# Kernel tuning notes

Hardware: AMD Instinct MI355X
Metric: run time of the kernel (lower is better)

## Reference

```python
import jax, jax.numpy as jnp
import numpy as np

# dims
B, T = 128, 1024
INP, HUMAN = 54, 64          # input_dim, output_dim (HUMAN_SIZE)
DEC, ENC = 256, 256          # decoder / encoder GRU sizes
K, H_PSI, LR_PSI = 16, 256, 32
N_PSI = DEC*DEC + DEC + DEC*INP + DEC*HUMAN + INP*(HUMAN-INP)  # 96540


def setup_inputs() -> dict:
    key = jax.random.key(0)
    ks = jax.random.split(key, 16)
    g = lambda i, shape, s=0.05: jax.random.normal(ks[i], shape, jnp.float32) * s
    return {
        "inputs": g(0, (B, T, INP), 1.0),
        "state": jnp.zeros((B, DEC), jnp.float32),
        "eps": g(1, (B, K), 1.0),
        # encoder GRUCell params (torch gate order r,z,n)
        "enc_Wih": g(2, (3*ENC, INP)),
        "enc_Whh": g(3, (3*ENC, ENC)),
        "enc_bih": jnp.zeros((3*ENC,), jnp.float32),
        "enc_bhh": jnp.zeros((3*ENC,), jnp.float32),
        # latent projections
        "to_mu": g(4, (K, ENC)),
        "to_lsigma": g(5, (K, ENC)),
        # psi hypernetwork MLP
        "W1": g(6, (H_PSI, K)),   "b1": jnp.zeros((H_PSI,), jnp.float32),
        "W2": g(7, (LR_PSI, H_PSI)), "b2": jnp.zeros((LR_PSI,), jnp.float32),
        "W3": g(8, (N_PSI, LR_PSI), 0.01), "b3": jnp.zeros((N_PSI,), jnp.float32),
        # shared decoder gate params (bias second half init to ones, as in module)
        "gru_Wih": g(9, (2*DEC, INP)),
        "gru_Whh": g(10, (DEC, 2*DEC)),
        "gru_bias": jnp.concatenate([jnp.zeros((DEC,)), jnp.ones((DEC,))]).astype(jnp.float32),
    }


def reference(inputs, state, eps, enc_Wih, enc_Whh, enc_bih, enc_bhh,
              to_mu, to_lsigma, W1, b1, W2, b2, W3, b3,
              gru_Wih, gru_Whh, gru_bias):
    x_tbd = jnp.swapaxes(inputs, 0, 1)  # [T,B,INP]

    # ---- encoder GRU scan (torch GRUCell semantics) ----
    def enc_step(h, x_t):
        gi = x_t @ enc_Wih.T + enc_bih
        gh = h @ enc_Whh.T + enc_bhh
        ir, iz, inn = jnp.split(gi, 3, axis=-1)
        hr, hz, hn = jnp.split(gh, 3, axis=-1)
        r = jax.nn.sigmoid(ir + hr)
        z = jax.nn.sigmoid(iz + hz)
        n = jnp.tanh(inn + r * hn)
        return (1 - z) * n + z * h, None

    h_enc, _ = jax.lax.scan(enc_step, jnp.zeros((inputs.shape[0], ENC), inputs.dtype), x_tbd)

    # ---- MT latent ----
    mu = h_enc @ to_mu.T                 # [B,K]
    logstd = h_enc @ to_lsigma.T         # [B,K]
    z_lat = mu + eps * jnp.exp(logstd)

    # ---- psi hypernetwork ----
    psi = jnp.tanh(z_lat @ W1.T + b1) @ W2.T + b2
    psi = psi @ W3.T + b3                # [B, N_PSI]

    o = 0
    Whh_p = psi[:, o:o+DEC*DEC].reshape(-1, DEC, DEC); o += DEC*DEC
    bh_p  = psi[:, o:o+DEC];                           o += DEC
    Wih_p = psi[:, o:o+DEC*INP].reshape(-1, DEC, INP); o += DEC*INP
    C_p   = psi[:, o:o+DEC*HUMAN].reshape(-1, DEC, HUMAN); o += DEC*HUMAN
    D_p   = psi[:, o:o+INP*(HUMAN-INP)].reshape(-1, INP, HUMAN-INP)

    # ---- per-sample hypernet-weighted GRU decoder, vectorized over batch ----
    def dec_step(h, x_t):  # h:[B,DEC], x_t:[B,INP]
        gx = x_t @ gru_Wih.T                       # [B,2*DEC]
        gh = h @ gru_Whh                           # [B,2*DEC]
        zt = jax.nn.sigmoid(gx[:, :DEC] + gh[:, :DEC] + gru_bias[:DEC])
        rt = jax.nn.sigmoid(gx[:, DEC:] + gh[:, DEC:] + gru_bias[DEC:])
        eta = jnp.tanh(jnp.einsum('bd,bhd->bh', x_t, Wih_p)
                       + rt * jnp.tanh(jnp.einsum('bh,bhg->bg', h, Whh_p) + bh_p))
        h_new = zt * h + (1 - zt) * eta
        return h_new, h_new

    h_last, dec_seq = jax.lax.scan(dec_step, state, x_tbd)
    dec_seq = jnp.swapaxes(dec_seq, 0, 1)          # [B,T,DEC]

    # yhat = dec@C + cat(zeros, x@D) ; residual adds inputs to first INP cols
    yD = jnp.einsum('btd,bde->bte', inputs, D_p)   # [B,T,HUMAN-INP]
    yhats = jnp.einsum('bth,bho->bto', dec_seq, C_p) + jnp.concatenate([inputs, yD], axis=-1)

    return yhats, mu, logstd, h_last
```

## Files before the change

### kernel.cpp

```cpp
#include <hip/hip_runtime.h>

#define BB 128
#define TT 1024
#define INP 54
#define HUM 64
#define NPSI 96540
#define OFF_BH 65536
#define OFF_WIH 65792
#define OFF_C 79616
#define OFF_D 96000
#define OUT_MU 8388608
#define OUT_LS 8390656
#define OUT_HL 8392704

typedef unsigned int u32;
typedef unsigned short u16;
typedef _Float16 h2 __attribute__((ext_vector_type(2)));

__device__ __forceinline__ u32 pk(float a, float b) {
    h2 v; v.x = (_Float16)a; v.y = (_Float16)b;
    return __builtin_bit_cast(u32, v);
}
__device__ __forceinline__ float f16tof(u16 v) {
    return (float)__builtin_bit_cast(_Float16, v);
}
__device__ __forceinline__ u16 ftof16(float v) {
    return __builtin_bit_cast(u16, (_Float16)v);
}
__device__ __forceinline__ float lo16f(u32 v) { return f16tof((u16)(v & 0xffffu)); }
__device__ __forceinline__ float hi16f(u32 v) { return f16tof((u16)(v >> 16)); }
__device__ __forceinline__ h2 bch2(u32 a) { return __builtin_bit_cast(h2, a); }
__device__ __forceinline__ float fd2(u32 a, u32 b, float c) {
#if __has_builtin(__builtin_amdgcn_fdot2)
    return __builtin_amdgcn_fdot2(bch2(a), bch2(b), c, false);
#else
    return c + lo16f(a) * lo16f(b) + hi16f(a) * hi16f(b);
#endif
}
__device__ __forceinline__ float fsig(float x) { return 1.f / (1.f + __expf(-x)); }
__device__ __forceinline__ float ftanh(float x) { float e = __expf(2.f * x); return 1.f - 2.f / (e + 1.f); }

__device__ __forceinline__ float qred(float v) {
#if __has_builtin(__builtin_amdgcn_mov_dpp)
    int x = __builtin_bit_cast(int, v);
    v += __builtin_bit_cast(float, __builtin_amdgcn_mov_dpp(x, 0xB1, 0xF, 0xF, true));
    x = __builtin_bit_cast(int, v);
    v += __builtin_bit_cast(float, __builtin_amdgcn_mov_dpp(x, 0x4E, 0xF, 0xF, true));
    return v;
#else
    v += __shfl_xor(v, 1); v += __shfl_xor(v, 2);
    return v;
#endif
}

__global__ __launch_bounds__(768, 3) void gemm_x_kernel(
    const float* __restrict__ inp, const float* __restrict__ W0,
    const u16* __restrict__ psi16, int mode, int t0, int len, int ct, int nt,
    u16* __restrict__ gout)
{
    const int tid = threadIdx.x;
    const int b = blockIdx.x / nt, tc = blockIdx.x % nt;
    const int gr = tid;
    float w[INP];
    if (mode == 0 || gr < 512) {
        const float* wsrc = W0 + (size_t)gr * INP;
#pragma unroll
        for (int c = 0; c < INP; ++c) w[c] = wsrc[c];
    } else {
        const u16* wsrc = psi16 + (size_t)b * NPSI + OFF_WIH + (size_t)(gr - 512) * INP;
#pragma unroll
        for (int c = 0; c < INP; ++c) w[c] = f16tof(wsrc[c]);
    }
    const int tb = tc * 128;
    const int te = (tb + 128 < len) ? tb + 128 : len;
    for (int tl = tb; tl < te; ++tl) {
        const float* xr = inp + ((size_t)b * TT + t0 + tl) * INP;
        float a = 0.f;
#pragma unroll
        for (int c = 0; c < INP; ++c) a = __builtin_fmaf(xr[c], w[c], a);
        gout[((size_t)b * ct + tl) * 768 + gr] = ftof16(a);
    }
}

__global__ __launch_bounds__(512) __attribute__((amdgpu_waves_per_eu(2, 2)))
void enc_scan_kernel(
    const u16* __restrict__ gi, int t0, int len, int ct,
    const float* __restrict__ Whh, const float* __restrict__ bih,
    const float* __restrict__ bhh, float* __restrict__ hcarry)
{
    __shared__ __align__(16) u32 hpp[2][144];
    const int tid = threadIdx.x, b = blockIdx.x;
    const int l = tid & 3, g = tid >> 2;
    const int j0 = 2 * g, j1 = 2 * g + 1;

    u32 wr0[32], wz0[32], wn0[32], wr1[32], wz1[32], wn1[32];
    {
        const float* pr0 = Whh + (size_t)j0 * 256 + 64 * l;
        const float* pz0 = Whh + (size_t)(256 + j0) * 256 + 64 * l;
        const float* pn0 = Whh + (size_t)(512 + j0) * 256 + 64 * l;
        const float* pr1 = Whh + (size_t)j1 * 256 + 64 * l;
        const float* pz1 = Whh + (size_t)(256 + j1) * 256 + 64 * l;
        const float* pn1 = Whh + (size_t)(512 + j1) * 256 + 64 * l;
#pragma unroll
        for (int c = 0; c < 32; ++c) {
            wr0[c] = pk(pr0[2 * c], pr0[2 * c + 1]);
            wz0[c] = pk(pz0[2 * c], pz0[2 * c + 1]);
            wn0[c] = pk(pn0[2 * c], pn0[2 * c + 1]);
            wr1[c] = pk(pr1[2 * c], pr1[2 * c + 1]);
            wz1[c] = pk(pz1[2 * c], pz1[2 * c + 1]);
            wn1[c] = pk(pn1[2 * c], pn1[2 * c + 1]);
        }
    }
    const float brb0 = bih[j0] + bhh[j0],             brb1 = bih[j1] + bhh[j1];
    const float bzb0 = bih[256 + j0] + bhh[256 + j0], bzb1 = bih[256 + j1] + bhh[256 + j1];
    const float bib0 = bih[512 + j0],                 bib1 = bih[512 + j1];
    const float bhb0 = bhh[512 + j0],                 bhb1 = bhh[512 + j1];
    float hc0 = 0.f, hc1 = 0.f;
    if (t0 > 0) { hc0 = hcarry[(size_t)b * 256 + j0]; hc1 = hcarry[(size_t)b * 256 + j1]; }
    if (tid < 128) {
        u32 hv = 0u;
        if (t0 > 0) hv = pk(hcarry[(size_t)b * 256 + 2 * tid], hcarry[(size_t)b * 256 + 2 * tid + 1]);
        hpp[0][36 * (tid >> 5) + (tid & 31)] = hv;
    }
    __syncthreads();

    const u16* gbase = gi + (size_t)b * ct * 768;
    u32 c0 = *(const u32*)(gbase + 2 * g);
    u32 c1 = *(const u32*)(gbase + 256 + 2 * g);
    u32 c2 = *(const u32*)(gbase + 512 + 2 * g);

    for (int tl = 0; tl < len; ++tl) {
        const int p = tl & 1;
        u32 n0 = 0, n1 = 0, n2 = 0;
        if (tl + 1 < len) {
            const u16* gn = gbase + (size_t)(tl + 1) * 768;
            n0 = *(const u32*)(gn + 2 * g);
            n1 = *(const u32*)(gn + 256 + 2 * g);
            n2 = *(const u32*)(gn + 512 + 2 * g);
        }
        float ar0 = 0, az0 = 0, ah0 = 0, ar1 = 0, az1 = 0, ah1 = 0;
        const uint4* hq = (const uint4*)hpp[p];
#pragma unroll
        for (int cc = 0; cc < 8; ++cc) {
            uint4 q = hq[9 * l + cc];
            u32 qa[4] = {q.x, q.y, q.z, q.w};
#pragma unroll
            for (int u = 0; u < 4; ++u) {
                const int c = cc * 4 + u;
                ar0 = fd2(wr0[c], qa[u], ar0);
                az0 = fd2(wz0[c], qa[u], az0);
                ah0 = fd2(wn0[c], qa[u], ah0);
                ar1 = fd2(wr1[c], qa[u], ar1);
                az1 = fd2(wz1[c], qa[u], az1);
                ah1 = fd2(wn1[c], qa[u], ah1);
            }
        }
        ar0 = qred(ar0); az0 = qred(az0); ah0 = qred(ah0);
        ar1 = qred(ar1); az1 = qred(az1); ah1 = qred(ah1);
        {
            float r0 = fsig(ar0 + lo16f(c0) + brb0);
            float z0 = fsig(az0 + lo16f(c1) + bzb0);
            float nn0 = ftanh(lo16f(c2) + bib0 + r0 * (ah0 + bhb0));
            float hn0 = (1.f - z0) * nn0 + z0 * hc0;
            float r1 = fsig(ar1 + hi16f(c0) + brb1);
            float z1 = fsig(az1 + hi16f(c1) + bzb1);
            float nn1 = ftanh(hi16f(c2) + bib1 + r1 * (ah1 + bhb1));
            float hn1 = (1.f - z1) * nn1 + z1 * hc1;
            hc0 = hn0; hc1 = hn1;
            if (l == 0) hpp[p ^ 1][36 * (g >> 5) + (g & 31)] = pk(hn0, hn1);
        }
        c0 = n0; c1 = n1; c2 = n2;
        __syncthreads();
    }
    if (l == 0) {
        hcarry[(size_t)b * 256 + j0] = hc0;
        hcarry[(size_t)b * 256 + j1] = hc1;
    }
}

__global__ __launch_bounds__(256) void latent_kernel(
    const float* __restrict__ henc, const float* __restrict__ eps,
    const float* __restrict__ to_mu, const float* __restrict__ to_ls,
    const float* __restrict__ W1, const float* __restrict__ b1,
    const float* __restrict__ W2, const float* __restrict__ b2,
    float* __restrict__ psi2, float* __restrict__ out)
{
    __shared__ float h[256], zz[16], p1[256];
    const int tid = threadIdx.x, b = blockIdx.x;
    h[tid] = henc[(size_t)b * 256 + tid];
    __syncthreads();
    if (tid < 16) {
        float m = 0, s = 0;
        for (int k = 0; k < 256; ++k) {
            m += h[k] * to_mu[tid * 256 + k];
            s += h[k] * to_ls[tid * 256 + k];
        }
        out[OUT_MU + b * 16 + tid] = m;
        out[OUT_LS + b * 16 + tid] = s;
        zz[tid] = m + eps[b * 16 + tid] * __expf(s);
    }
    __syncthreads();
    {
        float a = b1[tid];
        for (int k = 0; k < 16; ++k) a += zz[k] * W1[tid * 16 + k];
        p1[tid] = ftanh(a);
    }
    __syncthreads();
    if (tid < 32) {
        float a = b2[tid];
        for (int k = 0; k < 256; ++k) a += p1[k] * W2[tid * 256 + k];
        psi2[b * 32 + tid] = a;
    }
}

__global__ __launch_bounds__(256) void psi3_kernel(
    const float* __restrict__ psi2, const float* __restrict__ W3,
    const float* __restrict__ b3, u16* __restrict__ psi16)
{
    __shared__ float sp2[128 * 32];
    __shared__ float w3t[256 * 33];
    const int tid = threadIdx.x;
    const int n0 = blockIdx.x * 256;
    for (int idx = tid; idx < 4096; idx += 256) sp2[idx] = psi2[idx];
    for (int idx = tid; idx < 8192; idx += 256) {
        int row = idx >> 5, k = idx & 31;
        int n = n0 + row;
        w3t[row * 33 + k] = (n < NPSI) ? W3[(size_t)n * 32 + k] : 0.f;
    }
    __syncthreads();
    const int n = n0 + tid;
    if (n < NPSI) {
        float w[32];
#pragma unroll
        for (int k = 0; k < 32; ++k) w[k] = w3t[tid * 33 + k];
        const float bv = b3[n];
        for (int bi = 0; bi < 128; ++bi) {
            float a = bv;
#pragma unroll
            for (int k = 0; k < 32; ++k) a += sp2[bi * 32 + k] * w[k];
            psi16[(size_t)bi * NPSI + n] = ftof16(a);
        }
    }
}

__global__ __launch_bounds__(512) __attribute__((amdgpu_waves_per_eu(2, 2)))
void dec_scan_kernel(
    const u16* __restrict__ gx, int t0, int len, int ct,
    const float* __restrict__ state, const float* __restrict__ gWhh,
    const float* __restrict__ gbias, const u16* __restrict__ psi16,
    float* __restrict__ dcarry, float* __restrict__ out)
{
    __shared__ __align__(16) u32 hpp[2][144];
    __shared__ u32 cp[64 * 129];
    __shared__ float part[2][8 * 64];
    const int tid = threadIdx.x, b = blockIdx.x;
    const int l = tid & 3, g = tid >> 2;
    const int j0 = 2 * g, j1 = 2 * g + 1;
    const u16* pc = psi16 + (size_t)b * NPSI;

    u32 wz0[32], wr0[32], wp0[32], wz1[32], wr1[32], wp1[32];
#pragma unroll
    for (int c = 0; c < 32; ++c) {
        const int h0 = 64 * l + 2 * c;
        wz0[c] = pk(gWhh[(size_t)h0 * 512 + j0], gWhh[(size_t)(h0 + 1) * 512 + j0]);
        wr0[c] = pk(gWhh[(size_t)h0 * 512 + 256 + j0], gWhh[(size_t)(h0 + 1) * 512 + 256 + j0]);
        wp0[c] = (u32)pc[(size_t)h0 * 256 + j0] | ((u32)pc[(size_t)(h0 + 1) * 256 + j0] << 16);
        wz1[c] = pk(gWhh[(size_t)h0 * 512 + j1], gWhh[(size_t)(h0 + 1) * 512 + j1]);
        wr1[c] = pk(gWhh[(size_t)h0 * 512 + 256 + j1], gWhh[(size_t)(h0 + 1) * 512 + 256 + j1]);
        wp1[c] = (u32)pc[(size_t)h0 * 256 + j1] | ((u32)pc[(size_t)(h0 + 1) * 256 + j1] << 16);
    }
    const float gzb0 = gbias[j0], gzb1 = gbias[j1];
    const float grb0 = gbias[256 + j0], grb1 = gbias[256 + j1];
    const float bhb0 = f16tof(pc[OFF_BH + j0]), bhb1 = f16tof(pc[OFF_BH + j1]);
    for (int idx = tid; idx < 8192; idx += 512) {
        const int q = idx >> 6, o = idx & 63;
        cp[o * 129 + q] = (u32)pc[OFF_C + (size_t)(2 * q) * 64 + o]
                        | ((u32)pc[OFF_C + (size_t)(2 * q + 1) * 64 + o] << 16);
    }
    const float* hsrc = (t0 == 0) ? state : dcarry;
    float hc0 = hsrc[(size_t)b * 256 + j0];
    float hc1 = hsrc[(size_t)b * 256 + j1];
    if (tid < 128) hpp[0][36 * (tid >> 5) + (tid & 31)] =
        pk(hsrc[(size_t)b * 256 + 2 * tid], hsrc[(size_t)b * 256 + 2 * tid + 1]);
    __syncthreads();

    const u16* gbase = gx + (size_t)b * ct * 768;
    const int o = tid & 63, s = tid >> 6;
    const int hqi = 36 * (s >> 1) + 16 * (s & 1);
    u32 c0 = *(const u32*)(gbase + 2 * g);
    u32 c1 = *(const u32*)(gbase + 256 + 2 * g);
    u32 c2 = *(const u32*)(gbase + 512 + 2 * g);

    for (int tl = 0; tl < len; ++tl) {
        const int p = tl & 1;
        u32 n0 = 0, n1 = 0, n2 = 0;
        if (tl + 1 < len) {
            const u16* gn = gbase + (size_t)(tl + 1) * 768;
            n0 = *(const u32*)(gn + 2 * g);
            n1 = *(const u32*)(gn + 256 + 2 * g);
            n2 = *(const u32*)(gn + 512 + 2 * g);
        }
        {
            const uint4* h2q = (const uint4*)&hpp[p][hqi];
            uint4 qa = h2q[0], qb = h2q[1], qc = h2q[2], qd = h2q[3];
            u32 hv[16] = {qa.x, qa.y, qa.z, qa.w, qb.x, qb.y, qb.z, qb.w,
                          qc.x, qc.y, qc.z, qc.w, qd.x, qd.y, qd.z, qd.w};
            const int cbase = o * 129 + s * 16;
            float p0 = 0.f, p1 = 0.f;
#pragma unroll
            for (int i = 0; i < 8; ++i) {
                p0 = fd2(hv[2 * i], cp[cbase + 2 * i], p0);
                p1 = fd2(hv[2 * i + 1], cp[cbase + 2 * i + 1], p1);
            }
            part[p][s * 64 + o] = p0 + p1;
        }
        float az0 = 0, ar0 = 0, ap0 = 0, az1 = 0, ar1 = 0, ap1 = 0;
        const uint4* hq = (const uint4*)hpp[p];
#pragma unroll
        for (int cc = 0; cc < 8; ++cc) {
            uint4 q = hq[9 * l + cc];
            u32 qa[4] = {q.x, q.y, q.z, q.w};
#pragma unroll
            for (int u = 0; u < 4; ++u) {
                const int c = cc * 4 + u;
                az0 = fd2(wz0[c], qa[u], az0);
                ar0 = fd2(wr0[c], qa[u], ar0);
                ap0 = fd2(wp0[c], qa[u], ap0);
                az1 = fd2(wz1[c], qa[u], az1);
                ar1 = fd2(wr1[c], qa[u], ar1);
                ap1 = fd2(wp1[c], qa[u], ap1);
            }
        }
        az0 = qred(az0); ar0 = qred(ar0); ap0 = qred(ap0);
        az1 = qred(az1); ar1 = qred(ar1); ap1 = qred(ap1);
        {
            float zt0 = fsig(az0 + lo16f(c0) + gzb0);
            float rt0 = fsig(ar0 + lo16f(c1) + grb0);
            float eta0 = ftanh(lo16f(c2) + rt0 * ftanh(ap0 + bhb0));
            float hn0 = zt0 * hc0 + (1.f - zt0) * eta0;
            float zt1 = fsig(az1 + hi16f(c0) + gzb1);
            float rt1 = fsig(ar1 + hi16f(c1) + grb1);
            float eta1 = ftanh(hi16f(c2) + rt1 * ftanh(ap1 + bhb1));
            float hn1 = zt1 * hc1 + (1.f - zt1) * eta1;
            hc0 = hn0; hc1 = hn1;
            if (l == 0) hpp[p ^ 1][36 * (g >> 5) + (g & 31)] = pk(hn0, hn1);
        }
        if (tid < 64 && tl >= 2) {
            float y = 0.f;
#pragma unroll
            for (int s2 = 0; s2 < 8; ++s2) y += part[p ^ 1][s2 * 64 + tid];
            out[((size_t)b * TT + t0 + tl - 2) * HUM + tid] = y;
        }
        c0 = n0; c1 = n1; c2 = n2;
        __syncthreads();
    }
    {
        const int pf = (len - 1) & 1;
        if (tid < 64 && len >= 2) {
            float y = 0.f;
#pragma unroll
            for (int s2 = 0; s2 < 8; ++s2) y += part[pf][s2 * 64 + tid];
            out[((size_t)b * TT + t0 + len - 2) * HUM + tid] = y;
        }
        const int pl = len & 1;
        {
            const uint4* h2q = (const uint4*)&hpp[pl][hqi];
            uint4 qa = h2q[0], qb = h2q[1], qc = h2q[2], qd = h2q[3];
            u32 hv[16] = {qa.x, qa.y, qa.z, qa.w, qb.x, qb.y, qb.z, qb.w,
                          qc.x, qc.y, qc.z, qc.w, qd.x, qd.y, qd.z, qd.w};
            const int cbase = o * 129 + s * 16;
            float p0 = 0.f, p1 = 0.f;
#pragma unroll
            for (int i = 0; i < 8; ++i) {
                p0 = fd2(hv[2 * i], cp[cbase + 2 * i], p0);
                p1 = fd2(hv[2 * i + 1], cp[cbase + 2 * i + 1], p1);
            }
            part[pl][s * 64 + o] = p0 + p1;
        }
        __syncthreads();
        if (tid < 64) {
            float y = 0.f;
#pragma unroll
            for (int s2 = 0; s2 < 8; ++s2) y += part[pl][s2 * 64 + tid];
            out[((size_t)b * TT + t0 + len - 1) * HUM + tid] = y;
        }
    }
    if (l == 0) {
        dcarry[(size_t)b * 256 + j0] = hc0;
        dcarry[(size_t)b * 256 + j1] = hc1;
        if (t0 + len == TT) {
            out[OUT_HL + (size_t)b * 256 + j0] = hc0;
            out[OUT_HL + (size_t)b * 256 + j1] = hc1;
        }
    }
}

__global__ __launch_bounds__(256) void post_kernel(
    const float* __restrict__ inp, const u16* __restrict__ psi16,
    float* __restrict__ out)
{
    __shared__ float xs[128][55];
    __shared__ float ds[INP][10];
    const int tid = threadIdx.x;
    const int b = blockIdx.x >> 3, tile = blockIdx.x & 7;
    const int t0 = tile * 128;
    const u16* pc = psi16 + (size_t)b * NPSI;
    for (int idx = tid; idx < 540; idx += 256)
        ds[idx / 10][idx % 10] = f16tof(pc[OFF_D + idx]);
    for (int idx = tid; idx < 128 * INP; idx += 256) {
        const int t = idx / INP, d = idx % INP;
        xs[t][d] = inp[((size_t)b * TT + t0 + t) * INP + d];
    }
    __syncthreads();
    for (int i = 0; i < 32; ++i) {
        const int flat = i * 256 + tid;
        const int t = flat >> 6, o = flat & 63;
        const size_t oi = ((size_t)b * TT + t0 + t) * HUM + o;
        float y = out[oi];
        if (o < INP) y += xs[t][o];
        else {
            float acc = 0.f;
            for (int d = 0; d < INP; ++d) acc += xs[t][d] * ds[d][o - INP];
            y += acc;
        }
        out[oi] = y;
    }
}

extern "C" void kernel_launch(void* const* d_in, const int* in_sizes, int n_in,
                              void* d_out, int out_size, void* d_ws, size_t ws_size,
                              hipStream_t stream)
{
    const float* inputs = (const float*)d_in[0];
    const float* state  = (const float*)d_in[1];
    const float* eps    = (const float*)d_in[2];
    const float* eWih   = (const float*)d_in[3];
    const float* eWhh   = (const float*)d_in[4];
    const float* ebih   = (const float*)d_in[5];
    const float* ebhh   = (const float*)d_in[6];
    const float* to_mu  = (const float*)d_in[7];
    const float* to_ls  = (const float*)d_in[8];
    const float* W1     = (const float*)d_in[9];
    const float* b1     = (const float*)d_in[10];
    const float* W2     = (const float*)d_in[11];
    const float* b2     = (const float*)d_in[12];
    const float* W3     = (const float*)d_in[13];
    const float* b3     = (const float*)d_in[14];
    const float* gWih   = (const float*)d_in[15];
    const float* gWhh   = (const float*)d_in[16];
    const float* gbias  = (const float*)d_in[17];
    float* out = (float*)d_out;
    float* ws  = (float*)d_ws;

    float* henc   = ws;
    float* psi2   = ws + 32768;
    float* dcarry = ws + 36864;
    u16*   psi16  = (u16*)(ws + 69632);
    u16*   gbuf   = (u16*)(ws + 6248192);
    const size_t used = (size_t)6248192 * 4;
    size_t avail = (ws_size > used + 4096) ? (ws_size - used - 4096) : 0;
    int ct = (int)(avail / ((size_t)BB * 768 * 2));
    if (ct > TT) ct = TT;
    if (ct < 1) ct = 1;

    for (int t0 = 0; t0 < TT; t0 += ct) {
        const int len = (TT - t0 < ct) ? (TT - t0) : ct;
        const int nt = (len + 127) / 128;
        gemm_x_kernel<<<BB * nt, 768, 0, stream>>>(inputs, eWih, psi16, 0, t0, len, ct, nt, gbuf);
        enc_scan_kernel<<<BB, 512, 0, stream>>>(gbuf, t0, len, ct, eWhh, ebih, ebhh, henc);
    }
    latent_kernel<<<BB, 256, 0, stream>>>(henc, eps, to_mu, to_ls, W1, b1, W2, b2, psi2, out);
    psi3_kernel<<<(NPSI + 255) / 256, 256, 0, stream>>>(psi2, W3, b3, psi16);
    for (int t0 = 0; t0 < TT; t0 += ct) {
        const int len = (TT - t0 < ct) ? (TT - t0) : ct;
        const int nt = (len + 127) / 128;
        gemm_x_kernel<<<BB * nt, 768, 0, stream>>>(inputs, gWih, psi16, 1, t0, len, ct, nt, gbuf);
        dec_scan_kernel<<<BB, 512, 0, stream>>>(gbuf, t0, len, ct, state, gWhh, gbias, psi16, dcarry, out);
    }
    post_kernel<<<BB * 8, 256, 0, stream>>>(inputs, psi16, out);
}
```

Before: 3.944 ms.

## Move yhat projection out of decoder scan, stage gate inputs in LDS, packed-half encoder

The decoder scan no longer computes the per-step C projection inline. It writes each step's packed-half hidden state to a workspace sequence, and a new parallel yhat_kernel computes dec_seq@C across all timesteps afterwards. Both scans now stage precomputed input-gate values for 8 steps at a time into double-buffered LDS, replacing per-step global loads. The encoder dot products use packed fp16 FMA accumulators in place of fdot2 into fp32. This shortens the serial critical path, but adds a 64 MB hidden-state round trip, extra LDS traffic, and lower fp16 accumulation precision in the encoder.

```diff
diff --git a/kernel.cpp b/kernel.cpp
--- a/kernel.cpp
+++ b/kernel.cpp
@@ -37,6 +37,10 @@
     return c + lo16f(a) * lo16f(b) + hi16f(a) * hi16f(b);
 #endif
 }
+__device__ __forceinline__ h2 pfma(u32 a, u32 b, h2 c) {
+    return bch2(a) * bch2(b) + c;
+}
+__device__ __forceinline__ float h2tof(h2 s) { return (float)s.x + (float)s.y; }
 __device__ __forceinline__ float fsig(float x) { return 1.f / (1.f + __expf(-x)); }
 __device__ __forceinline__ float ftanh(float x) { float e = __expf(2.f * x); return 1.f - 2.f / (e + 1.f); }
 
@@ -89,6 +93,7 @@
     const float* __restrict__ bhh, float* __restrict__ hcarry)
 {
     __shared__ __align__(16) u32 hpp[2][144];
+    __shared__ __align__(16) u32 gxs[2][3072];
     const int tid = threadIdx.x, b = blockIdx.x;
     const int l = tid & 3, g = tid >> 2;
     const int j0 = 2 * g, j1 = 2 * g + 1;
@@ -122,55 +127,93 @@
         if (t0 > 0) hv = pk(hcarry[(size_t)b * 256 + 2 * tid], hcarry[(size_t)b * 256 + 2 * tid + 1]);
         hpp[0][36 * (tid >> 5) + (tid & 31)] = hv;
     }
-    __syncthreads();
-
-    const u16* gbase = gi + (size_t)b * ct * 768;
-    u32 c0 = *(const u32*)(gbase + 2 * g);
-    u32 c1 = *(const u32*)(gbase + 256 + 2 * g);
-    u32 c2 = *(const u32*)(gbase + 512 + 2 * g);
-
-    for (int tl = 0; tl < len; ++tl) {
-        const int p = tl & 1;
-        u32 n0 = 0, n1 = 0, n2 = 0;
-        if (tl + 1 < len) {
-            const u16* gn = gbase + (size_t)(tl + 1) * 768;
-            n0 = *(const u32*)(gn + 2 * g);
-            n1 = *(const u32*)(gn + 256 + 2 * g);
-            n2 = *(const u32*)(gn + 512 + 2 * g);
-        }
-        float ar0 = 0, az0 = 0, ah0 = 0, ar1 = 0, az1 = 0, ah1 = 0;
-        const uint4* hq = (const uint4*)hpp[p];
-#pragma unroll
-        for (int cc = 0; cc < 8; ++cc) {
-            uint4 q = hq[9 * l + cc];
-            u32 qa[4] = {q.x, q.y, q.z, q.w};
-#pragma unroll
-            for (int u = 0; u < 4; ++u) {
-                const int c = cc * 4 + u;
-                ar0 = fd2(wr0[c], qa[u], ar0);
-                az0 = fd2(wz0[c], qa[u], az0);
-                ah0 = fd2(wn0[c], qa[u], ah0);
-                ar1 = fd2(wr1[c], qa[u], ar1);
-                az1 = fd2(wz1[c], qa[u], az1);
-                ah1 = fd2(wn1[c], qa[u], ah1);
-            }
-        }
-        ar0 = qred(ar0); az0 = qred(az0); ah0 = qred(ah0);
-        ar1 = qred(ar1); az1 = qred(az1); ah1 = qred(ah1);
-        {
-            float r0 = fsig(ar0 + lo16f(c0) + brb0);
-            float z0 = fsig(az0 + lo16f(c1) + bzb0);
-            float nn0 = ftanh(lo16f(c2) + bib0 + r0 * (ah0 + bhb0));
-            float hn0 = (1.f - z0) * nn0 + z0 * hc0;
-            float r1 = fsig(ar1 + hi16f(c0) + brb1);
-            float z1 = fsig(az1 + hi16f(c1) + bzb1);
-            float nn1 = ftanh(hi16f(c2) + bib1 + r1 * (ah1 + bhb1));
-            float hn1 = (1.f - z1) * nn1 + z1 * hc1;
-            hc0 = hn0; hc1 = hn1;
-            if (l == 0) hpp[p ^ 1][36 * (g >> 5) + (g & 31)] = pk(hn0, hn1);
-        }
-        c0 = n0; c1 = n1; c2 = n2;
+    const u32* gb32 = (const u32*)(gi + (size_t)b * ct * 768);
+    {
+        const int steps0 = (len < 8) ? len : 8;
+#pragma unroll
+        for (int k = 0; k < 6; ++k) {
+            const int f = k * 512 + tid;
+            if (f < 384 * steps0) gxs[0][f] = gb32[f];
+        }
+    }
+    __syncthreads();
+
+    const h2 z2 = {(_Float16)0.f, (_Float16)0.f};
+    int buf = 0;
+    for (int cb = 0; cb < len; cb += 8) {
+        const int steps = (len - cb < 8) ? (len - cb) : 8;
+        const int nsteps = (len - cb - 8 < 8) ? (len - cb - 8) : 8;
+        u32 stg[6];
+        if (nsteps > 0) {
+            const u32* gsrc = gb32 + (size_t)(cb + 8) * 384;
+#pragma unroll
+            for (int k = 0; k < 6; ++k) {
+                const int f = k * 512 + tid;
+                if (f < 384 * nsteps) stg[k] = gsrc[f];
+            }
+        }
+        for (int st = 0; st < steps; ++st) {
+            const int tl = cb + st;
+            const int p = tl & 1;
+            const u32 c0 = gxs[buf][st * 384 + g];
+            const u32 c1 = gxs[buf][st * 384 + 128 + g];
+            const u32 c2 = gxs[buf][st * 384 + 256 + g];
+            h2 vr0a = z2, vr0b = z2, vz0a = z2, vz0b = z2, vn0a = z2, vn0b = z2;
+            h2 vr1a = z2, vr1b = z2, vz1a = z2, vz1b = z2, vn1a = z2, vn1b = z2;
+            const uint4* hq = (const uint4*)hpp[p];
+#pragma unroll
+            for (int cc = 0; cc < 8; ++cc) {
+                uint4 q = hq[9 * l + cc];
+                u32 qa[4] = {q.x, q.y, q.z, q.w};
+#pragma unroll
+                for (int u = 0; u < 4; ++u) {
+                    const int c = cc * 4 + u;
+                    if (u & 1) {
+                        vr0b = pfma(wr0[c], qa[u], vr0b);
+                        vz0b = pfma(wz0[c], qa[u], vz0b);
+                        vn0b = pfma(wn0[c], qa[u], vn0b);
+                        vr1b = pfma(wr1[c], qa[u], vr1b);
+                        vz1b = pfma(wz1[c], qa[u], vz1b);
+                        vn1b = pfma(wn1[c], qa[u], vn1b);
+                    } else {
+                        vr0a = pfma(wr0[c], qa[u], vr0a);
+                        vz0a = pfma(wz0[c], qa[u], vz0a);
+                        vn0a = pfma(wn0[c], qa[u], vn0a);
+                        vr1a = pfma(wr1[c], qa[u], vr1a);
+                        vz1a = pfma(wz1[c], qa[u], vz1a);
+                        vn1a = pfma(wn1[c], qa[u], vn1a);
+                    }
+                }
+            }
+            float ar0 = qred(h2tof(vr0a + vr0b));
+            float az0 = qred(h2tof(vz0a + vz0b));
+            float ah0 = qred(h2tof(vn0a + vn0b));
+            float ar1 = qred(h2tof(vr1a + vr1b));
+            float az1 = qred(h2tof(vz1a + vz1b));
+            float ah1 = qred(h2tof(vn1a + vn1b));
+            {
+                float r0 = fsig(ar0 + lo16f(c0) + brb0);
+                float z0 = fsig(az0 + lo16f(c1) + bzb0);
+                float nn0 = ftanh(lo16f(c2) + bib0 + r0 * (ah0 + bhb0));
+                float hn0 = (1.f - z0) * nn0 + z0 * hc0;
+                float r1 = fsig(ar1 + hi16f(c0) + brb1);
+                float z1 = fsig(az1 + hi16f(c1) + bzb1);
+                float nn1 = ftanh(hi16f(c2) + bib1 + r1 * (ah1 + bhb1));
+                float hn1 = (1.f - z1) * nn1 + z1 * hc1;
+                hc0 = hn0; hc1 = hn1;
+                if (l == 0) hpp[p ^ 1][36 * (g >> 5) + (g & 31)] = pk(hn0, hn1);
+            }
+            __syncthreads();
+        }
+        if (nsteps > 0) {
+#pragma unroll
+            for (int k = 0; k < 6; ++k) {
+                const int f = k * 512 + tid;
+                if (f < 384 * nsteps) gxs[buf ^ 1][f] = stg[k];
+            }
+        }
         __syncthreads();
+        buf ^= 1;
     }
     if (l == 0) {
         hcarry[(size_t)b * 256 + j0] = hc0;
@@ -248,11 +291,10 @@
     const u16* __restrict__ gx, int t0, int len, int ct,
     const float* __restrict__ state, const float* __restrict__ gWhh,
     const float* __restrict__ gbias, const u16* __restrict__ psi16,
-    float* __restrict__ dcarry, float* __restrict__ out)
+    float* __restrict__ dcarry, u32* __restrict__ hseq, float* __restrict__ out)
 {
     __shared__ __align__(16) u32 hpp[2][144];
-    __shared__ u32 cp[64 * 129];
-    __shared__ float part[2][8 * 64];
+    __shared__ __align__(16) u32 gxs[2][3072];
     const int tid = threadIdx.x, b = blockIdx.x;
     const int l = tid & 3, g = tid >> 2;
     const int j0 = 2 * g, j1 = 2 * g + 1;
@@ -272,118 +314,88 @@
     const float gzb0 = gbias[j0], gzb1 = gbias[j1];
     const float grb0 = gbias[256 + j0], grb1 = gbias[256 + j1];
     const float bhb0 = f16tof(pc[OFF_BH + j0]), bhb1 = f16tof(pc[OFF_BH + j1]);
-    for (int idx = tid; idx < 8192; idx += 512) {
-        const int q = idx >> 6, o = idx & 63;
-        cp[o * 129 + q] = (u32)pc[OFF_C + (size_t)(2 * q) * 64 + o]
-                        | ((u32)pc[OFF_C + (size_t)(2 * q + 1) * 64 + o] << 16);
-    }
     const float* hsrc = (t0 == 0) ? state : dcarry;
     float hc0 = hsrc[(size_t)b * 256 + j0];
     float hc1 = hsrc[(size_t)b * 256 + j1];
     if (tid < 128) hpp[0][36 * (tid >> 5) + (tid & 31)] =
         pk(hsrc[(size_t)b * 256 + 2 * tid], hsrc[(size_t)b * 256 + 2 * tid + 1]);
-    __syncthreads();
-
-    const u16* gbase = gx + (size_t)b * ct * 768;
-    const int o = tid & 63, s = tid >> 6;
-    const int hqi = 36 * (s >> 1) + 16 * (s & 1);
-    u32 c0 = *(const u32*)(gbase + 2 * g);
-    u32 c1 = *(const u32*)(gbase + 256 + 2 * g);
-    u32 c2 = *(const u32*)(gbase + 512 + 2 * g);
-
-    for (int tl = 0; tl < len; ++tl) {
-        const int p = tl & 1;
-        u32 n0 = 0, n1 = 0, n2 = 0;
-        if (tl + 1 < len) {
-            const u16* gn = gbase + (size_t)(tl + 1) * 768;
-            n0 = *(const u32*)(gn + 2 * g);
-            n1 = *(const u32*)(gn + 256 + 2 * g);
-            n2 = *(const u32*)(gn + 512 + 2 * g);
-        }
-        {
-            const uint4* h2q = (const uint4*)&hpp[p][hqi];
-            uint4 qa = h2q[0], qb = h2q[1], qc = h2q[2], qd = h2q[3];
-            u32 hv[16] = {qa.x, qa.y, qa.z, qa.w, qb.x, qb.y, qb.z, qb.w,
-                          qc.x, qc.y, qc.z, qc.w, qd.x, qd.y, qd.z, qd.w};
-            const int cbase = o * 129 + s * 16;
-            float p0 = 0.f, p1 = 0.f;
-#pragma unroll
-            for (int i = 0; i < 8; ++i) {
-                p0 = fd2(hv[2 * i], cp[cbase + 2 * i], p0);
-                p1 = fd2(hv[2 * i + 1], cp[cbase + 2 * i + 1], p1);
-            }
-            part[p][s * 64 + o] = p0 + p1;
-        }
-        float az0 = 0, ar0 = 0, ap0 = 0, az1 = 0, ar1 = 0, ap1 = 0;
-        const uint4* hq = (const uint4*)hpp[p];
-#pragma unroll
-        for (int cc = 0; cc < 8; ++cc) {
-            uint4 q = hq[9 * l + cc];
-            u32 qa[4] = {q.x, q.y, q.z, q.w};
-#pragma unroll
-            for (int u = 0; u < 4; ++u) {
-                const int c = cc * 4 + u;
-                az0 = fd2(wz0[c], qa[u], az0);
-                ar0 = fd2(wr0[c], qa[u], ar0);
-                ap0 = fd2(wp0[c], qa[u], ap0);
-                az1 = fd2(wz1[c], qa[u], az1);
-                ar1 = fd2(wr1[c], qa[u], ar1);
-                ap1 = fd2(wp1[c], qa[u], ap1);
-            }
-        }
-        az0 = qred(az0); ar0 = qred(ar0); ap0 = qred(ap0);
-        az1 = qred(az1); ar1 = qred(ar1); ap1 = qred(ap1);
-        {
-            float zt0 = fsig(az0 + lo16f(c0) + gzb0);
-            float rt0 = fsig(ar0 + lo16f(c1) + grb0);
-            float eta0 = ftanh(lo16f(c2) + rt0 * ftanh(ap0 + bhb0));
-            float hn0 = zt0 * hc0 + (1.f - zt0) * eta0;
-            float zt1 = fsig(az1 + hi16f(c0) + gzb1);
-            float rt1 = fsig(ar1 + hi16f(c1) + grb1);
-            float eta1 = ftanh(hi16f(c2) + rt1 * ftanh(ap1 + bhb1));
-            float hn1 = zt1 * hc1 + (1.f - zt1) * eta1;
-            hc0 = hn0; hc1 = hn1;
-            if (l == 0) hpp[p ^ 1][36 * (g >> 5) + (g & 31)] = pk(hn0, hn1);
-        }
-        if (tid < 64 && tl >= 2) {
-            float y = 0.f;
-#pragma unroll
-            for (int s2 = 0; s2 < 8; ++s2) y += part[p ^ 1][s2 * 64 + tid];
-            out[((size_t)b * TT + t0 + tl - 2) * HUM + tid] = y;
-        }
-        c0 = n0; c1 = n1; c2 = n2;
+    const u32* gb32 = (const u32*)(gx + (size_t)b * ct * 768);
+    {
+        const int steps0 = (len < 8) ? len : 8;
+#pragma unroll
+        for (int k = 0; k < 6; ++k) {
+            const int f = k * 512 + tid;
+            if (f < 384 * steps0) gxs[0][f] = gb32[f];
+        }
+    }
+    __syncthreads();
+
+    u32* hsb = hseq + (size_t)b * TT * 128;
+    int buf = 0;
+    for (int cb = 0; cb < len; cb += 8) {
+        const int steps = (len - cb < 8) ? (len - cb) : 8;
+        const int nsteps = (len - cb - 8 < 8) ? (len - cb - 8) : 8;
+        u32 stg[6];
+        if (nsteps > 0) {
+            const u32* gsrc = gb32 + (size_t)(cb + 8) * 384;
+#pragma unroll
+            for (int k = 0; k < 6; ++k) {
+                const int f = k * 512 + tid;
+                if (f < 384 * nsteps) stg[k] = gsrc[f];
+            }
+        }
+        for (int st = 0; st < steps; ++st) {
+            const int tl = cb + st;
+            const int p = tl & 1;
+            const u32 c0 = gxs[buf][st * 384 + g];
+            const u32 c1 = gxs[buf][st * 384 + 128 + g];
+            const u32 c2 = gxs[buf][st * 384 + 256 + g];
+            float az0 = 0, ar0 = 0, ap0 = 0, az1 = 0, ar1 = 0, ap1 = 0;
+            const uint4* hq = (const uint4*)hpp[p];
+#pragma unroll
+            for (int cc = 0; cc < 8; ++cc) {
+                uint4 q = hq[9 * l + cc];
+                u32 qa[4] = {q.x, q.y, q.z, q.w};
+#pragma unroll
+                for (int u = 0; u < 4; ++u) {
+                    const int c = cc * 4 + u;
+                    az0 = fd2(wz0[c], qa[u], az0);
+                    ar0 = fd2(wr0[c], qa[u], ar0);
+                    ap0 = fd2(wp0[c], qa[u], ap0);
+                    az1 = fd2(wz1[c], qa[u], az1);
+                    ar1 = fd2(wr1[c], qa[u], ar1);
+                    ap1 = fd2(wp1[c], qa[u], ap1);
+                }
+            }
+            az0 = qred(az0); ar0 = qred(ar0); ap0 = qred(ap0);
+            az1 = qred(az1); ar1 = qred(ar1); ap1 = qred(ap1);
+            {
+                float zt0 = fsig(az0 + lo16f(c0) + gzb0);
+                float rt0 = fsig(ar0 + lo16f(c1) + grb0);
+                float eta0 = ftanh(lo16f(c2) + rt0 * ftanh(ap0 + bhb0));
+                float hn0 = zt0 * hc0 + (1.f - zt0) * eta0;
+                float zt1 = fsig(az1 + hi16f(c0) + gzb1);
+                float rt1 = fsig(ar1 + hi16f(c1) + grb1);
+                float eta1 = ftanh(hi16f(c2) + rt1 * ftanh(ap1 + bhb1));
+                float hn1 = zt1 * hc1 + (1.f - zt1) * eta1;
+                hc0 = hn0; hc1 = hn1;
+                if (l == 0) {
+                    u32 hv = pk(hn0, hn1);
+                    hpp[p ^ 1][36 * (g >> 5) + (g & 31)] = hv;
+                    hsb[(size_t)(t0 + tl) * 128 + g] = hv;
+                }
+            }
+            __syncthreads();
+        }
+        if (nsteps > 0) {
+#pragma unroll
+            for (int k = 0; k < 6; ++k) {
+                const int f = k * 512 + tid;
+                if (f < 384 * nsteps) gxs[buf ^ 1][f] = stg[k];
+            }
+        }
         __syncthreads();
-    }
-    {
-        const int pf = (len - 1) & 1;
-        if (tid < 64 && len >= 2) {
-            float y = 0.f;
-#pragma unroll
-            for (int s2 = 0; s2 < 8; ++s2) y += part[pf][s2 * 64 + tid];
-            out[((size_t)b * TT + t0 + len - 2) * HUM + tid] = y;
-        }
-        const int pl = len & 1;
-        {
-            const uint4* h2q = (const uint4*)&hpp[pl][hqi];
-            uint4 qa = h2q[0], qb = h2q[1], qc = h2q[2], qd = h2q[3];
-            u32 hv[16] = {qa.x, qa.y, qa.z, qa.w, qb.x, qb.y, qb.z, qb.w,
-                          qc.x, qc.y, qc.z, qc.w, qd.x, qd.y, qd.z, qd.w};
-            const int cbase = o * 129 + s * 16;
-            float p0 = 0.f, p1 = 0.f;
-#pragma unroll
-            for (int i = 0; i < 8; ++i) {
-                p0 = fd2(hv[2 * i], cp[cbase + 2 * i], p0);
-                p1 = fd2(hv[2 * i + 1], cp[cbase + 2 * i + 1], p1);
-            }
-            part[pl][s * 64 + o] = p0 + p1;
-        }
-        __syncthreads();
-        if (tid < 64) {
-            float y = 0.f;
-#pragma unroll
-            for (int s2 = 0; s2 < 8; ++s2) y += part[pl][s2 * 64 + tid];
-            out[((size_t)b * TT + t0 + len - 1) * HUM + tid] = y;
-        }
+        buf ^= 1;
     }
     if (l == 0) {
         dcarry[(size_t)b * 256 + j0] = hc0;
@@ -392,6 +404,46 @@
             out[OUT_HL + (size_t)b * 256 + j0] = hc0;
             out[OUT_HL + (size_t)b * 256 + j1] = hc1;
         }
+    }
+}
+
+#define YT 32
+__global__ __launch_bounds__(256) void yhat_kernel(
+    const u32* __restrict__ hseq, const u16* __restrict__ psi16,
+    float* __restrict__ out)
+{
+    __shared__ float part[2][YT][64];
+    const int tid = threadIdx.x;
+    const int b = blockIdx.x >> 5, tile = blockIdx.x & 31;
+    const int o = tid & 63, s = (tid >> 6) & 1, tq = tid >> 7;
+    const u16* pc = psi16 + (size_t)b * NPSI;
+    u32 cpr[64];
+#pragma unroll
+    for (int i = 0; i < 64; ++i) {
+        const int gp = s * 64 + i;
+        cpr[i] = (u32)pc[OFF_C + (size_t)(2 * gp) * 64 + o]
+               | ((u32)pc[OFF_C + (size_t)(2 * gp + 1) * 64 + o] << 16);
+    }
+    const int t0 = tile * YT;
+    for (int th = 0; th < YT / 2; ++th) {
+        const int tl = tq * (YT / 2) + th;
+        const uint4* h4 = (const uint4*)(hseq + ((size_t)b * TT + t0 + tl) * 128 + s * 64);
+        float a = 0.f;
+#pragma unroll
+        for (int gc = 0; gc < 16; ++gc) {
+            uint4 q = h4[gc];
+            a = fd2(q.x, cpr[gc * 4 + 0], a);
+            a = fd2(q.y, cpr[gc * 4 + 1], a);
+            a = fd2(q.z, cpr[gc * 4 + 2], a);
+            a = fd2(q.w, cpr[gc * 4 + 3], a);
+        }
+        part[s][tl][o] = a;
+    }
+    __syncthreads();
+    for (int i = 0; i < 8; ++i) {
+        const int flat = i * 256 + tid;
+        const int tl = flat >> 6, o2 = flat & 63;
+        out[((size_t)b * TT + t0 + tl) * HUM + o2] = part[0][tl][o2] + part[1][tl][o2];
     }
 }
 
@@ -456,8 +508,9 @@
     float* psi2   = ws + 32768;
     float* dcarry = ws + 36864;
     u16*   psi16  = (u16*)(ws + 69632);
-    u16*   gbuf   = (u16*)(ws + 6248192);
-    const size_t used = (size_t)6248192 * 4;
+    u32*   hseq   = (u32*)(ws + 6248192);
+    u16*   gbuf   = (u16*)(ws + 23025408);
+    const size_t used = (size_t)23025408 * 4;
     size_t avail = (ws_size > used + 4096) ? (ws_size - used - 4096) : 0;
     int ct = (int)(avail / ((size_t)BB * 768 * 2));
     if (ct > TT) ct = TT;
@@ -475,7 +528,9 @@
         const int len = (TT - t0 < ct) ? (TT - t0) : ct;
         const int nt = (len + 127) / 128;
         gemm_x_kernel<<<BB * nt, 768, 0, stream>>>(inputs, gWih, psi16, 1, t0, len, ct, nt, gbuf);
-        dec_scan_kernel<<<BB, 512, 0, stream>>>(gbuf, t0, len, ct, state, gWhh, gbias, psi16, dcarry, out);
-    }
+        dec_scan_kernel<<<BB, 512, 0, stream>>>(gbuf, t0, len, ct, state, gWhh, gbias, psi16,
+                                                dcarry, hseq, out);
+    }
+    yhat_kernel<<<BB * 32, 256, 0, stream>>>(hseq, psi16, out);
     post_kernel<<<BB * 8, 256, 0, stream>>>(inputs, psi16, out);
 }
```

Measured after the change: 4.706 ms. 1.19x slower.
